# Kernel optimization log

Measured on AMD Instinct MI355X. Metric: run time of the kernel, lower is better.

The kernel has to match this reference:

```python
import jax, jax.numpy as jnp
import numpy as np

N = 100000   # num_nodes
E = 3200000  # num_edges
F = 7        # node_features
H = 128      # hidden_dim
D = 64       # embedding_dim
EPS = 1e-5


def setup_inputs() -> dict:
    key = jax.random.key(0)
    ks = jax.random.split(key, 32)
    inp = {}
    inp["x"] = jax.random.normal(ks[0], (N, F), jnp.float32)
    inp["edge_index"] = jax.random.randint(ks[1], (2, E), 0, N, dtype=jnp.int64)
    # input projection
    inp["W_in"] = jax.random.normal(ks[2], (F, H), jnp.float32) * 0.1
    inp["b_in"] = jax.random.normal(ks[3], (H,), jnp.float32) * 0.01
    # 3 GCN layers: 128->128, 128->128, 128->64, each with eval-mode BatchNorm params
    dims = [(H, H), (H, H), (H, D)]
    for i, (di, do) in enumerate(dims):
        k = jax.random.split(ks[4 + i], 6)
        inp[f"W{i}"] = jax.random.normal(k[0], (di, do), jnp.float32) * (1.0 / np.sqrt(di))
        inp[f"b{i}"] = jax.random.normal(k[1], (do,), jnp.float32) * 0.01
        inp[f"g{i}"] = 1.0 + 0.1 * jax.random.normal(k[2], (do,), jnp.float32)
        inp[f"be{i}"] = 0.1 * jax.random.normal(k[3], (do,), jnp.float32)
        inp[f"m{i}"] = 0.1 * jax.random.normal(k[4], (do,), jnp.float32)
        inp[f"v{i}"] = jax.random.uniform(k[5], (do,), jnp.float32, 0.5, 1.5)
    return inp


def _gcn_conv(x, W, b, src, dst, dinv):
    h = x @ W                                   # [N, do]
    coef = dinv[src] * dinv[dst]                # [E]
    agg = jax.ops.segment_sum(h[src] * coef[:, None], dst, num_segments=N)
    # self-loop contribution: norm = dinv[i]^2
    return agg + h * (dinv * dinv)[:, None] + b


def _bn_eval(x, g, be, m, v):
    return (x - m) * (g * jax.lax.rsqrt(v + EPS)) + be


def reference(x, edge_index, W_in, b_in,
              W0, b0, g0, be0, m0, v0,
              W1, b1, g1, be1, m1, v1,
              W2, b2, g2, be2, m2, v2):
    src, dst = edge_index[0], edge_index[1]
    # in-degree with self-loops (same for all layers)
    deg = jax.ops.segment_sum(jnp.ones((E,), x.dtype), dst, num_segments=N) + 1.0
    dinv = jax.lax.rsqrt(deg)

    h = jax.nn.relu(x @ W_in + b_in)            # [N, H]

    # layer 0: conv -> bn -> relu -> (dropout=id, eval) -> residual
    h0 = _gcn_conv(h, W0, b0, src, dst, dinv)
    h0 = jax.nn.relu(_bn_eval(h0, g0, be0, m0, v0)) + h
    # layer 1
    h1 = _gcn_conv(h0, W1, b1, src, dst, dinv)
    h1 = jax.nn.relu(_bn_eval(h1, g1, be1, m1, v1)) + h0
    # layer 2 (final): conv -> bn only (shape changes to D, no residual/relu)
    h2 = _gcn_conv(h1, W2, b2, src, dst, dinv)
    return _bn_eval(h2, g2, be2, m2, v2)        # [N, D]
```

## Files before the change

kernel.cpp:

```cpp
#include <hip/hip_runtime.h>


#define NN 100000
#define NE 3200000
#define FI 7
#define HD 128
#define DD 64
#define EPS 1e-5f
#define NB 196
#define EPB 8192
#define NBLK ((NE + EPB - 1) / EPB)
#define EMAX 20000

typedef float float2v __attribute__((ext_vector_type(2)));
typedef short short8 __attribute__((ext_vector_type(8)));
typedef float f32x4 __attribute__((ext_vector_type(4)));

__device__ __forceinline__ unsigned char f2fp8(float f) {
    return (unsigned char)(__builtin_amdgcn_cvt_pk_fp8_f32(f, f, 0, false) & 0xFF);
}
__device__ __forceinline__ unsigned short f2bf(float f) {
    unsigned u = __float_as_uint(f);
    u += 0x7FFF + ((u >> 16) & 1);
    return (unsigned short)(u >> 16);
}


__global__ __launch_bounds__(256) void pA_bin(const int* __restrict__ ei,
                                              int* __restrict__ bcnt,
                                              int* __restrict__ ebin) {
    __shared__ int sdst[EPB];
    __shared__ int hcur[NB];
    const int t = threadIdx.x;
    for (int b = t; b < NB; b += 256) hcur[b] = 0;
    __syncthreads();
    const int base = blockIdx.x * EPB;
    const int cnt = min(EPB, NE - base);
    for (int i = t; i < cnt; i += 256) {
        int d = ei[NE + base + i];
        sdst[i] = d;
        atomicAdd(&hcur[d >> 9], 1);
    }
    __syncthreads();
    for (int b = t; b < NB; b += 256) {
        int c = hcur[b];
        hcur[b] = (c ? atomicAdd(&bcnt[b], c) : 0) + b * EMAX;
    }
    __syncthreads();
    for (int i = t; i < cnt; i += 256) {
        int s = ei[base + i];
        int d = sdst[i];
        int p = atomicAdd(&hcur[d >> 9], 1);
        ebin[p] = ((d & 511) << 23) | s;
    }
}

__global__ __launch_bounds__(512) void p4_finalize(const int* __restrict__ bcnt,
                                                   const int* __restrict__ ebin,
                                                   int* __restrict__ esrc,
                                                   int* __restrict__ rowstart,
                                                   float* __restrict__ dinv) {
    __shared__ int sh[256];
    __shared__ int lh[512];
    __shared__ int sc[512];
    __shared__ int lc[512];
    const int t = threadIdx.x;
    const int b = blockIdx.x;
    if (t < 256) sh[t] = (t < NB) ? bcnt[t] : 0;
    __syncthreads();
    for (int off = 1; off < 256; off <<= 1) {
        int v = (t < 256 && t >= off) ? sh[t - off] : 0;
        __syncthreads();
        if (t < 256) sh[t] += v;
        __syncthreads();
    }
    const int ecnt = bcnt[b];
    const int ebase = sh[b] - ecnt;
    const int rbase = b * EMAX;
    const int n0 = b << 9;
    lh[t] = 0;
    __syncthreads();
    for (int i = t; i < ecnt; i += 512)
        atomicAdd(&lh[((unsigned)ebin[rbase + i]) >> 23], 1);
    __syncthreads();
    const int c = lh[t];
    sc[t] = c;
    __syncthreads();
    for (int off = 1; off < 512; off <<= 1) {
        int v = (t >= off) ? sc[t - off] : 0;
        __syncthreads();
        sc[t] += v;
        __syncthreads();
    }
    const int excl = ebase + sc[t] - c;
    lc[t] = excl;
    const int node = n0 + t;
    if (node < NN) {
        rowstart[node] = excl;
        dinv[node] = rsqrtf((float)c + 1.0f);
    }
    if (b == NB - 1 && t == 0) rowstart[NN] = NE;
    __syncthreads();
    for (int i = t; i < ecnt; i += 512) {
        int v = ebin[rbase + i];
        int p = atomicAdd(&lc[((unsigned)v) >> 23], 1);
        esrc[p] = v & 0x7FFFFF;
    }
}


__global__ __launch_bounds__(256) void inproj_kernel(const float* __restrict__ x,
                                                     const float* __restrict__ W_in,
                                                     const float* __restrict__ b_in,
                                                     float* __restrict__ hA,
                                                     unsigned short* __restrict__ hAbf) {
    int n = blockIdx.x * 2 + (threadIdx.x >> 7);
    int j = threadIdx.x & 127;
    float acc = b_in[j];
#pragma unroll
    for (int f = 0; f < FI; ++f) acc += x[n * FI + f] * W_in[f * HD + j];
    acc = fmaxf(acc, 0.f);
    hA[n * HD + j] = acc;
    hAbf[n * HD + j] = f2bf(acc);
}


__global__ __launch_bounds__(64) void wprep_all(const float* __restrict__ W0,
                                                const float* __restrict__ W1,
                                                const float* __restrict__ W2,
                                                unsigned short* __restrict__ wf0,
                                                unsigned short* __restrict__ wf1,
                                                unsigned short* __restrict__ wf2) {
    const int blk = blockIdx.x;
    const float* W;
    unsigned short* Wf;
    int DO, rel;
    if (blk < 32) { W = W0; Wf = wf0; DO = 128; rel = blk; }
    else if (blk < 64) { W = W1; Wf = wf1; DO = 128; rel = blk - 32; }
    else { W = W2; Wf = wf2; DO = 64; rel = blk - 64; }
    const int lane = threadIdx.x;
    const int nt = rel >> 2;
    const int ks = rel & 3;
    short8 o;
#pragma unroll
    for (int j = 0; j < 8; ++j)
        o[j] = (short)f2bf(W[(ks * 32 + (lane >> 4) * 8 + j) * DO + nt * 16 + (lane & 15)]);
    *(short8*)(Wf + ((size_t)rel * 64 + lane) * 8) = o;
}


template <int DO>
__global__ __launch_bounds__(256) void gemm_mfma(const unsigned short* __restrict__ A,
                                                 const unsigned short* __restrict__ Wf,
                                                 const float* __restrict__ dinv,
                                                 unsigned char* __restrict__ B) {
    constexpr int CT = DO / 64;
    const int tid = threadIdx.x;
    const int wave = tid >> 6;
    const int lane = tid & 63;
    const int n0 = blockIdx.x * 32;
    short8 bfrag[CT][4];
#pragma unroll
    for (int ct = 0; ct < CT; ++ct)
#pragma unroll
        for (int ks = 0; ks < 4; ++ks)
            bfrag[ct][ks] = *(const short8*)(Wf + ((size_t)(((wave * CT + ct) * 4 + ks) * 64) + lane) * 8);
#pragma unroll
    for (int rt = 0; rt < 2; ++rt) {
        const int arow = n0 + rt * 16 + (lane & 15);
        short8 afrag[4];
#pragma unroll
        for (int ks = 0; ks < 4; ++ks)
            afrag[ks] = *(const short8*)(A + (size_t)arow * HD + ks * 32 + ((lane >> 4) & 3) * 8);
        f32x4 acc[CT];
#pragma unroll
        for (int ct = 0; ct < CT; ++ct) acc[ct] = (f32x4){0.f, 0.f, 0.f, 0.f};
#pragma unroll
        for (int ks = 0; ks < 4; ++ks)
#pragma unroll
            for (int ct = 0; ct < CT; ++ct)
                acc[ct] = __builtin_amdgcn_mfma_f32_16x16x32_bf16(afrag[ks], bfrag[ct][ks], acc[ct], 0, 0, 0);
#pragma unroll
        for (int r = 0; r < 4; ++r) {
            const int orow = n0 + rt * 16 + (lane >> 4) * 4 + r;
            const float dv = dinv[orow];
#pragma unroll
            for (int ct = 0; ct < CT; ++ct) {
                const int ocol = (wave * CT + ct) * 16 + (lane & 15);
                B[(size_t)orow * DO + ocol] = f2fp8(acc[ct][r] * dv);
            }
        }
    }
}


template <int DO, bool RELU_RES>
__global__ __launch_bounds__(128) void gather_kernel(const unsigned char* __restrict__ hXW,
                                                     float* __restrict__ resOut,
                                                     unsigned short* __restrict__ resBf,
                                                     const int* __restrict__ rowstart,
                                                     const int* __restrict__ esrc,
                                                     const float* __restrict__ dinv,
                                                     const float* __restrict__ bias,
                                                     const float* __restrict__ g,
                                                     const float* __restrict__ be,
                                                     const float* __restrict__ m,
                                                     const float* __restrict__ v) {
    constexpr int CG = DO / 8;
    constexpr int NG = 128 / CG;
    constexpr int QN = DO / 4;
    __shared__ int s_idx[128];
    __shared__ float sred[8][128];
    const int n = blockIdx.x;
    const int t = threadIdx.x;
    const int rs = rowstart[n];
    const int re = rowstart[n + 1];
    const float dn = dinv[n];
    const int q = t & (CG - 1);
    const int grp = t / CG;
    float4 a0l = {0.f, 0.f, 0.f, 0.f}, a0h = {0.f, 0.f, 0.f, 0.f};
    float4 a1l = {0.f, 0.f, 0.f, 0.f}, a1h = {0.f, 0.f, 0.f, 0.f};
    for (int base = rs; base < re; base += 128) {
        const int c = min(128, re - base);
        __syncthreads();
        if (t < c) s_idx[t] = esrc[base + t];
        __syncthreads();
        for (int j = grp; j < c; j += 2 * NG) {
            {
                const uint2 u = *(const uint2*)(hXW + (size_t)s_idx[j] * DO + q * 8);
                const float2v l0 = __builtin_amdgcn_cvt_pk_f32_fp8(u.x, false);
                const float2v h0 = __builtin_amdgcn_cvt_pk_f32_fp8(u.x, true);
                const float2v l1 = __builtin_amdgcn_cvt_pk_f32_fp8(u.y, false);
                const float2v h1 = __builtin_amdgcn_cvt_pk_f32_fp8(u.y, true);
                a0l.x += l0.x; a0l.y += l0.y; a0l.z += h0.x; a0l.w += h0.y;
                a0h.x += l1.x; a0h.y += l1.y; a0h.z += h1.x; a0h.w += h1.y;
            }
            if (j + NG < c) {
                const uint2 u = *(const uint2*)(hXW + (size_t)s_idx[j + NG] * DO + q * 8);
                const float2v l0 = __builtin_amdgcn_cvt_pk_f32_fp8(u.x, false);
                const float2v h0 = __builtin_amdgcn_cvt_pk_f32_fp8(u.x, true);
                const float2v l1 = __builtin_amdgcn_cvt_pk_f32_fp8(u.y, false);
                const float2v h1 = __builtin_amdgcn_cvt_pk_f32_fp8(u.y, true);
                a1l.x += l0.x; a1l.y += l0.y; a1l.z += h0.x; a1l.w += h0.y;
                a1h.x += l1.x; a1h.y += l1.y; a1h.z += h1.x; a1h.w += h1.y;
            }
        }
    }
    a0l.x += a1l.x; a0l.y += a1l.y; a0l.z += a1l.z; a0l.w += a1l.w;
    a0h.x += a1h.x; a0h.y += a1h.y; a0h.z += a1h.z; a0h.w += a1h.w;
    __syncthreads();
    sred[0][t] = a0l.x; sred[1][t] = a0l.y; sred[2][t] = a0l.z; sred[3][t] = a0l.w;
    sred[4][t] = a0h.x; sred[5][t] = a0h.y; sred[6][t] = a0h.z; sred[7][t] = a0h.w;
    __syncthreads();
    if (t < QN) {
        const int qq = t >> 1, h = t & 1;
        float4 sum = {0.f, 0.f, 0.f, 0.f};
#pragma unroll
        for (int k = 0; k < NG; ++k) {
            const int u = k * CG + qq;
            sum.x += sred[h * 4 + 0][u];
            sum.y += sred[h * 4 + 1][u];
            sum.z += sred[h * 4 + 2][u];
            sum.w += sred[h * 4 + 3][u];
        }
        const unsigned su = *(const unsigned*)(hXW + (size_t)n * DO + t * 4);
        const float2v slo = __builtin_amdgcn_cvt_pk_f32_fp8(su, false);
        const float2v shi = __builtin_amdgcn_cvt_pk_f32_fp8(su, true);
        const float4 b4 = *(const float4*)(bias + t * 4);
        const float4 g4 = *(const float4*)(g + t * 4);
        const float4 be4 = *(const float4*)(be + t * 4);
        const float4 m4 = *(const float4*)(m + t * 4);
        const float4 v4 = *(const float4*)(v + t * 4);
        float4 val;
        val.x = (sum.x + slo.x) * dn + b4.x;
        val.y = (sum.y + slo.y) * dn + b4.y;
        val.z = (sum.z + shi.x) * dn + b4.z;
        val.w = (sum.w + shi.y) * dn + b4.w;
        val.x = (val.x - m4.x) * (g4.x * rsqrtf(v4.x + EPS)) + be4.x;
        val.y = (val.y - m4.y) * (g4.y * rsqrtf(v4.y + EPS)) + be4.y;
        val.z = (val.z - m4.z) * (g4.z * rsqrtf(v4.z + EPS)) + be4.z;
        val.w = (val.w - m4.w) * (g4.w * rsqrtf(v4.w + EPS)) + be4.w;
        float4* outp = (float4*)(resOut + (size_t)n * DO + t * 4);
        if (RELU_RES) {
            const float4 r = *outp;
            val.x = fmaxf(val.x, 0.f) + r.x;
            val.y = fmaxf(val.y, 0.f) + r.y;
            val.z = fmaxf(val.z, 0.f) + r.z;
            val.w = fmaxf(val.w, 0.f) + r.w;
            ushort4 bf;
            bf.x = f2bf(val.x); bf.y = f2bf(val.y);
            bf.z = f2bf(val.z); bf.w = f2bf(val.w);
            *(ushort4*)(resBf + (size_t)n * DO + t * 4) = bf;
        }
        *outp = val;
    }
}


extern "C" void kernel_launch(void* const* d_in, const int* in_sizes, int n_in,
                              void* d_out, int out_size, void* d_ws, size_t ws_size,
                              hipStream_t stream) {
    const float* x    = (const float*)d_in[0];
    const int*   ei   = (const int*)d_in[1];
    const float* W_in = (const float*)d_in[2];
    const float* b_in = (const float*)d_in[3];
    const float* Wl[3] = {(const float*)d_in[4], (const float*)d_in[10], (const float*)d_in[16]};
    const float* bl[3] = {(const float*)d_in[5], (const float*)d_in[11], (const float*)d_in[17]};
    const float* gl[3] = {(const float*)d_in[6], (const float*)d_in[12], (const float*)d_in[18]};
    const float* bel[3] = {(const float*)d_in[7], (const float*)d_in[13], (const float*)d_in[19]};
    const float* ml[3] = {(const float*)d_in[8], (const float*)d_in[14], (const float*)d_in[20]};
    const float* vl[3] = {(const float*)d_in[9], (const float*)d_in[15], (const float*)d_in[21]};
    float* out = (float*)d_out;

    char* ws = (char*)d_ws;
    size_t off = 0;
    auto carve = [&](size_t bytes) {
        void* p = ws + off;
        off += (bytes + 255) & ~(size_t)255;
        return p;
    };
    int*   bcnt     = (int*)carve(NB * sizeof(int));
    int*   rowstart = (int*)carve((NN + 1) * sizeof(int));
    float* dinv     = (float*)carve(NN * sizeof(float));
    int*   esrc     = (int*)carve((size_t)NE * sizeof(int));
    float* hA       = (float*)carve((size_t)NN * HD * sizeof(float));
    unsigned short* hAbf = (unsigned short*)carve((size_t)NN * HD * sizeof(unsigned short));
    unsigned char* hB = (unsigned char*)carve((size_t)NN * HD);
    int*   ebin     = (int*)carve((size_t)NB * EMAX * sizeof(int));
    unsigned short* wf0 = (unsigned short*)carve((size_t)HD * HD * sizeof(unsigned short));
    unsigned short* wf1 = (unsigned short*)carve((size_t)HD * HD * sizeof(unsigned short));
    unsigned short* wf2 = (unsigned short*)carve((size_t)HD * DD * sizeof(unsigned short));
    (void)ws_size;

    hipMemsetAsync(bcnt, 0, NB * sizeof(int), stream);

    wprep_all<<<80, 64, 0, stream>>>(Wl[0], Wl[1], Wl[2], wf0, wf1, wf2);

    pA_bin<<<NBLK, 256, 0, stream>>>(ei, bcnt, ebin);
    p4_finalize<<<NB, 512, 0, stream>>>(bcnt, ebin, esrc, rowstart, dinv);

    inproj_kernel<<<NN / 2, 256, 0, stream>>>(x, W_in, b_in, hA, hAbf);

    gemm_mfma<128><<<NN / 32, 256, 0, stream>>>(hAbf, wf0, dinv, hB);
    gather_kernel<128, true><<<NN, 128, 0, stream>>>(hB, hA, hAbf, rowstart, esrc, dinv,
                                                     bl[0], gl[0], bel[0], ml[0], vl[0]);
    gemm_mfma<128><<<NN / 32, 256, 0, stream>>>(hAbf, wf1, dinv, hB);
    gather_kernel<128, true><<<NN, 128, 0, stream>>>(hB, hA, hAbf, rowstart, esrc, dinv,
                                                     bl[1], gl[1], bel[1], ml[1], vl[1]);
    gemm_mfma<64><<<NN / 32, 256, 0, stream>>>(hAbf, wf2, dinv, hB);
    gather_kernel<64, false><<<NN, 128, 0, stream>>>(hB, out, (unsigned short*)nullptr,
                                                     rowstart, esrc, dinv,
                                                     bl[2], gl[2], bel[2], ml[2], vl[2]);
}
```

Before: 513.2 us.

## Replace atomic bin reservation with per-block histogram and scan for deterministic binning

```diff
diff --git a/kernel.cpp b/kernel.cpp
--- a/kernel.cpp
+++ b/kernel.cpp
@@ -11,6 +11,7 @@
 #define EPB 8192
 #define NBLK ((NE + EPB - 1) / EPB)
 #define EMAX 20000
+#define WPREPB 20
 
 typedef float float2v __attribute__((ext_vector_type(2)));
 typedef short short8 __attribute__((ext_vector_type(8)));
@@ -26,31 +27,79 @@
 }
 
 
-__global__ __launch_bounds__(256) void pA_bin(const int* __restrict__ ei,
-                                              int* __restrict__ bcnt,
+__global__ __launch_bounds__(256) void pH_hist(const int* __restrict__ ei,
+                                               int* __restrict__ blk_off,
+                                               const float* __restrict__ W0,
+                                               const float* __restrict__ W1,
+                                               const float* __restrict__ W2,
+                                               unsigned short* __restrict__ wf0,
+                                               unsigned short* __restrict__ wf1,
+                                               unsigned short* __restrict__ wf2) {
+    const int t = threadIdx.x;
+    if (blockIdx.x >= NBLK) {
+        const int unit = (blockIdx.x - NBLK) * 4 + (t >> 6);
+        const int lane = t & 63;
+        const float* W;
+        unsigned short* Wf;
+        int DO, rel;
+        if (unit < 32) { W = W0; Wf = wf0; DO = 128; rel = unit; }
+        else if (unit < 64) { W = W1; Wf = wf1; DO = 128; rel = unit - 32; }
+        else { W = W2; Wf = wf2; DO = 64; rel = unit - 64; }
+        const int nt = rel >> 2;
+        const int ks = rel & 3;
+        short8 o;
+#pragma unroll
+        for (int j = 0; j < 8; ++j)
+            o[j] = (short)f2bf(W[(ks * 32 + (lane >> 4) * 8 + j) * DO + nt * 16 + (lane & 15)]);
+        *(short8*)(Wf + ((size_t)rel * 64 + lane) * 8) = o;
+        return;
+    }
+    __shared__ int h[NB];
+    for (int b = t; b < NB; b += 256) h[b] = 0;
+    __syncthreads();
+    const int base = blockIdx.x * EPB;
+    const int cnt = min(EPB, NE - base);
+    for (int i = t; i < cnt; i += 256)
+        atomicAdd(&h[ei[NE + base + i] >> 9], 1);
+    __syncthreads();
+    for (int b = t; b < NB; b += 256)
+        blk_off[blockIdx.x * NB + b] = h[b];
+}
+
+
+__global__ __launch_bounds__(512) void pS_scan(int* __restrict__ blk_off,
+                                               int* __restrict__ bcnt) {
+    __shared__ int sh[512];
+    const int t = threadIdx.x;
+    const int b = blockIdx.x;
+    const int myc = (t < NBLK) ? blk_off[t * NB + b] : 0;
+    sh[t] = myc;
+    __syncthreads();
+    for (int off = 1; off < 512; off <<= 1) {
+        int v = (t >= off) ? sh[t - off] : 0;
+        __syncthreads();
+        sh[t] += v;
+        __syncthreads();
+    }
+    if (t < NBLK) blk_off[t * NB + b] = sh[t] - myc;
+    if (t == NBLK - 1) bcnt[b] = sh[t];
+}
+
+
+__global__ __launch_bounds__(256) void pB_bin(const int* __restrict__ ei,
+                                              const int* __restrict__ blk_off,
                                               int* __restrict__ ebin) {
-    __shared__ int sdst[EPB];
-    __shared__ int hcur[NB];
-    const int t = threadIdx.x;
-    for (int b = t; b < NB; b += 256) hcur[b] = 0;
+    __shared__ int cur[NB];
+    const int t = threadIdx.x;
+    for (int b = t; b < NB; b += 256)
+        cur[b] = b * EMAX + blk_off[blockIdx.x * NB + b];
     __syncthreads();
     const int base = blockIdx.x * EPB;
     const int cnt = min(EPB, NE - base);
     for (int i = t; i < cnt; i += 256) {
+        int s = ei[base + i];
         int d = ei[NE + base + i];
-        sdst[i] = d;
-        atomicAdd(&hcur[d >> 9], 1);
-    }
-    __syncthreads();
-    for (int b = t; b < NB; b += 256) {
-        int c = hcur[b];
-        hcur[b] = (c ? atomicAdd(&bcnt[b], c) : 0) + b * EMAX;
-    }
-    __syncthreads();
-    for (int i = t; i < cnt; i += 256) {
-        int s = ei[base + i];
-        int d = sdst[i];
-        int p = atomicAdd(&hcur[d >> 9], 1);
+        int p = atomicAdd(&cur[d >> 9], 1);
         ebin[p] = ((d & 511) << 23) | s;
     }
 }
@@ -122,30 +171,6 @@
     acc = fmaxf(acc, 0.f);
     hA[n * HD + j] = acc;
     hAbf[n * HD + j] = f2bf(acc);
-}
-
-
-__global__ __launch_bounds__(64) void wprep_all(const float* __restrict__ W0,
-                                                const float* __restrict__ W1,
-                                                const float* __restrict__ W2,
-                                                unsigned short* __restrict__ wf0,
-                                                unsigned short* __restrict__ wf1,
-                                                unsigned short* __restrict__ wf2) {
-    const int blk = blockIdx.x;
-    const float* W;
-    unsigned short* Wf;
-    int DO, rel;
-    if (blk < 32) { W = W0; Wf = wf0; DO = 128; rel = blk; }
-    else if (blk < 64) { W = W1; Wf = wf1; DO = 128; rel = blk - 32; }
-    else { W = W2; Wf = wf2; DO = 64; rel = blk - 64; }
-    const int lane = threadIdx.x;
-    const int nt = rel >> 2;
-    const int ks = rel & 3;
-    short8 o;
-#pragma unroll
-    for (int j = 0; j < 8; ++j)
-        o[j] = (short)f2bf(W[(ks * 32 + (lane >> 4) * 8 + j) * DO + nt * 16 + (lane & 15)]);
-    *(short8*)(Wf + ((size_t)rel * 64 + lane) * 8) = o;
 }
 
 
@@ -218,6 +243,14 @@
     const float dn = dinv[n];
     const int q = t & (CG - 1);
     const int grp = t / CG;
+    unsigned su = 0;
+    float4 resv = {0.f, 0.f, 0.f, 0.f};
+    float4* outp = nullptr;
+    if (t < QN) {
+        su = *(const unsigned*)(hXW + (size_t)n * DO + t * 4);
+        outp = (float4*)(resOut + (size_t)n * DO + t * 4);
+        if (RELU_RES) resv = *outp;
+    }
     float4 a0l = {0.f, 0.f, 0.f, 0.f}, a0h = {0.f, 0.f, 0.f, 0.f};
     float4 a1l = {0.f, 0.f, 0.f, 0.f}, a1h = {0.f, 0.f, 0.f, 0.f};
     for (int base = rs; base < re; base += 128) {
@@ -263,7 +296,6 @@
             sum.z += sred[h * 4 + 2][u];
             sum.w += sred[h * 4 + 3][u];
         }
-        const unsigned su = *(const unsigned*)(hXW + (size_t)n * DO + t * 4);
         const float2v slo = __builtin_amdgcn_cvt_pk_f32_fp8(su, false);
         const float2v shi = __builtin_amdgcn_cvt_pk_f32_fp8(su, true);
         const float4 b4 = *(const float4*)(bias + t * 4);
@@ -280,13 +312,11 @@
         val.y = (val.y - m4.y) * (g4.y * rsqrtf(v4.y + EPS)) + be4.y;
         val.z = (val.z - m4.z) * (g4.z * rsqrtf(v4.z + EPS)) + be4.z;
         val.w = (val.w - m4.w) * (g4.w * rsqrtf(v4.w + EPS)) + be4.w;
-        float4* outp = (float4*)(resOut + (size_t)n * DO + t * 4);
         if (RELU_RES) {
-            const float4 r = *outp;
-            val.x = fmaxf(val.x, 0.f) + r.x;
-            val.y = fmaxf(val.y, 0.f) + r.y;
-            val.z = fmaxf(val.z, 0.f) + r.z;
-            val.w = fmaxf(val.w, 0.f) + r.w;
+            val.x = fmaxf(val.x, 0.f) + resv.x;
+            val.y = fmaxf(val.y, 0.f) + resv.y;
+            val.z = fmaxf(val.z, 0.f) + resv.z;
+            val.w = fmaxf(val.w, 0.f) + resv.w;
             ushort4 bf;
             bf.x = f2bf(val.x); bf.y = f2bf(val.y);
             bf.z = f2bf(val.z); bf.w = f2bf(val.w);
@@ -320,6 +350,7 @@
         return p;
     };
     int*   bcnt     = (int*)carve(NB * sizeof(int));
+    int*   blk_off  = (int*)carve((size_t)NBLK * NB * sizeof(int));
     int*   rowstart = (int*)carve((NN + 1) * sizeof(int));
     float* dinv     = (float*)carve(NN * sizeof(float));
     int*   esrc     = (int*)carve((size_t)NE * sizeof(int));
@@ -332,11 +363,10 @@
     unsigned short* wf2 = (unsigned short*)carve((size_t)HD * DD * sizeof(unsigned short));
     (void)ws_size;
 
-    hipMemsetAsync(bcnt, 0, NB * sizeof(int), stream);
-
-    wprep_all<<<80, 64, 0, stream>>>(Wl[0], Wl[1], Wl[2], wf0, wf1, wf2);
-
-    pA_bin<<<NBLK, 256, 0, stream>>>(ei, bcnt, ebin);
+    pH_hist<<<NBLK + WPREPB, 256, 0, stream>>>(ei, blk_off, Wl[0], Wl[1], Wl[2],
+                                               wf0, wf1, wf2);
+    pS_scan<<<NB, 512, 0, stream>>>(blk_off, bcnt);
+    pB_bin<<<NBLK, 256, 0, stream>>>(ei, blk_off, ebin);
     p4_finalize<<<NB, 512, 0, stream>>>(bcnt, ebin, esrc, rowstart, dinv);
 
     inproj_kernel<<<NN / 2, 256, 0, stream>>>(x, W_in, b_in, hA, hAbf);
```

Measured after the change: 514.0 us. About the same (+0.2%).
